# Optimization experiments

Hardware: AMD Instinct MI355X
Metric: run time of the kernel (lower is better)

Reference implementation:

```python
import jax, jax.numpy as jnp
import numpy as np

DIM = 256
HEADS = 8
HEAD_DIM = DIM // HEADS
B_, N = 8192, 49


def setup_inputs() -> dict:
    key = jax.random.key(0)
    k1, k2, k3, k4, k5, k6 = jax.random.split(key, 6)
    x = jax.random.normal(k1, (B_, N, DIM), dtype=jnp.float32)
    mask = jax.random.normal(k2, (B_, N, N), dtype=jnp.float32)
    s = 1.0 / np.sqrt(DIM)
    W_qkv = jax.random.normal(k3, (3 * DIM, DIM), dtype=jnp.float32) * s
    b_qkv = jax.random.normal(k4, (3 * DIM,), dtype=jnp.float32) * 0.02
    W_proj = jax.random.normal(k5, (DIM, DIM), dtype=jnp.float32) * s
    b_proj = jax.random.normal(k6, (DIM,), dtype=jnp.float32) * 0.02
    return {"x": x, "mask": mask, "W_qkv": W_qkv, "b_qkv": b_qkv,
            "W_proj": W_proj, "b_proj": b_proj}


def reference(x, mask, W_qkv, b_qkv, W_proj, b_proj):
    B, n, C = x.shape
    scale = HEAD_DIM ** (-0.5)
    # qkv projection: (B, N, 3C) -> (3, B, H, N, hd)
    qkv = x @ W_qkv.T + b_qkv
    qkv = qkv.reshape(B, n, 3, HEADS, HEAD_DIM).transpose(2, 0, 3, 1, 4)
    q, k, v = qkv[0], qkv[1], qkv[2]
    # scaled dot-product within each window
    attn = jnp.einsum('bhqd,bhkd->bhqk', q, k) * scale
    attn = attn + mask[:, None, :, :]  # additive window mask
    attn = jax.nn.softmax(attn, axis=-1)
    out = jnp.einsum('bhqk,bhkd->bhqd', attn, v)
    out = out.transpose(0, 2, 1, 3).reshape(B, n, C)
    return out @ W_proj.T + b_proj
```

## Files before the change

kernel.cpp:

```cpp
#include <hip/hip_runtime.h>
#include <hip/hip_bf16.h>

#define NTOK 49
#define DIMC 256

typedef __attribute__((ext_vector_type(8))) short bf16x8;
typedef __attribute__((ext_vector_type(4))) float f32x4;

static __device__ __forceinline__ unsigned pk2(float a, float b) {
    union { __hip_bfloat16 h; unsigned short u; } ua, ub;
    ua.h = __float2bfloat16(a);
    ub.h = __float2bfloat16(b);
    return (unsigned)ua.u | ((unsigned)ub.u << 16);
}

static __device__ __forceinline__ bf16x8 mkfrag(unsigned w0, unsigned w1, unsigned w2, unsigned w3) {
    union { bf16x8 v; unsigned u[4]; } t;
    t.u[0] = w0; t.u[1] = w1; t.u[2] = w2; t.u[3] = w3;
    return t.v;
}

static __device__ __forceinline__ unsigned sel2(unsigned lo, unsigned hi, int src, int ghi) {
    unsigned a = __shfl(lo, src);
    unsigned b = __shfl(hi, src);
    return ghi ? b : a;
}

__global__ void convert_weights(const float* __restrict__ wq, const float* __restrict__ wp,
                                unsigned short* __restrict__ wqb, unsigned short* __restrict__ wpb) {
    int i = blockIdx.x * 256 + threadIdx.x;
    if (i < 768 * 256) {
        union { __hip_bfloat16 h; unsigned short u; } t;
        t.h = __float2bfloat16(wq[i]);
        wqb[i] = t.u;
    }
    if (i < 256 * 256) {
        union { __hip_bfloat16 h; unsigned short u; } t;
        t.h = __float2bfloat16(wp[i]);
        wpb[i] = t.u;
    }
}

__launch_bounds__(512, 2)
__global__ void win_attn_fused(const float* __restrict__ x, const float* __restrict__ mask,
                               const unsigned short* __restrict__ wqb, const float* __restrict__ bqkv,
                               const unsigned short* __restrict__ wpb, const float* __restrict__ bproj,
                               float* __restrict__ out) {
    __shared__ __align__(16) char lds[49152];
    char* const xb = lds;
    char* const mb = lds + 32768;

    const int b = blockIdx.x;
    const int tid = threadIdx.x;
    const int lane = tid & 63;
    const int wid = tid >> 6;
    const int c = lane & 15;
    const int g = lane >> 4;

    const f32x4 fzero = {0.f, 0.f, 0.f, 0.f};

    {
        const float* xw = x + (size_t)b * (NTOK * DIMC);
        #pragma unroll
        for (int it = 0; it < 8; ++it) {
            int idx = it * 512 + tid;
            int t = idx >> 6;
            int d0 = (idx & 63) * 4;
            float4 v = make_float4(0.f, 0.f, 0.f, 0.f);
            if (t < NTOK) v = *(const float4*)(xw + t * DIMC + d0);
            *(uint2*)(xb + t * 512 + ((d0 * 2) ^ ((t & 7) << 4))) =
                make_uint2(pk2(v.x, v.y), pk2(v.z, v.w));
        }
        const float* mw = mask + (size_t)b * (NTOK * NTOK);
        #pragma unroll
        for (int it = 0; it < 8; ++it) {
            int idx = it * 512 + tid;
            int q = idx >> 6;
            int key = idx & 63;
            float v;
            if (q < NTOK && key < NTOK) v = mw[q * NTOK + key];
            else v = (key >= NTOK) ? -1e30f : 0.f;
            *(float*)(mb + q * 256 + ((key * 4) ^ ((q & 7) << 4))) = v;
        }
    }
    __syncthreads();

    const int h = wid;
    const int srcA = c + 16 * ((2 * g) & 3);
    const int srcB = c + 16 * ((2 * g + 1) & 3);
    const int ghi = g >> 1;
    const float scale = 0.17677669529663687f;

    #define XFRAG(t_, kk_) (*(const bf16x8*)(xb + (t_) * 512 + ((2 * ((kk_) + 8 * g)) ^ (((t_) & 7) << 4))))

    bf16x8 vf[2][2];
    {
        f32x4 acc[4][2];
        #pragma unroll
        for (int mt = 0; mt < 4; ++mt)
            #pragma unroll
            for (int j2 = 0; j2 < 2; ++j2) acc[mt][j2] = fzero;
        #pragma unroll
        for (int ks = 0; ks < 8; ++ks) {
            int kk = ks * 32;
            bf16x8 ax[4];
            #pragma unroll
            for (int mt = 0; mt < 4; ++mt) { int t = mt * 16 + c; ax[mt] = XFRAG(t, kk); }
            #pragma unroll
            for (int j2 = 0; j2 < 2; ++j2) {
                bf16x8 wb = *(const bf16x8*)(wqb + (512 + h * 32 + j2 * 16 + c) * 256 + kk + 8 * g);
                #pragma unroll
                for (int mt = 0; mt < 4; ++mt)
                    acc[mt][j2] = __builtin_amdgcn_mfma_f32_16x16x32_bf16(ax[mt], wb, acc[mt][j2], 0, 0, 0);
            }
        }
        float bv0 = bqkv[512 + h * 32 + c];
        float bv1 = bqkv[512 + h * 32 + 16 + c];
        unsigned vpp[4][2][2];
        #pragma unroll
        for (int mt = 0; mt < 4; ++mt) {
            vpp[mt][0][0] = pk2(acc[mt][0][0] + bv0, acc[mt][0][1] + bv0);
            vpp[mt][0][1] = pk2(acc[mt][0][2] + bv0, acc[mt][0][3] + bv0);
            vpp[mt][1][0] = pk2(acc[mt][1][0] + bv1, acc[mt][1][1] + bv1);
            vpp[mt][1][1] = pk2(acc[mt][1][2] + bv1, acc[mt][1][3] + bv1);
        }
        #pragma unroll
        for (int kh = 0; kh < 2; ++kh)
            #pragma unroll
            for (int dt = 0; dt < 2; ++dt)
                vf[kh][dt] = mkfrag(sel2(vpp[2 * kh][dt][0], vpp[2 * kh + 1][dt][0], srcA, ghi),
                                    sel2(vpp[2 * kh][dt][1], vpp[2 * kh + 1][dt][1], srcA, ghi),
                                    sel2(vpp[2 * kh][dt][0], vpp[2 * kh + 1][dt][0], srcB, ghi),
                                    sel2(vpp[2 * kh][dt][1], vpp[2 * kh + 1][dt][1], srcB, ghi));
    }

    bf16x8 ka[4];
    {
        f32x4 acc[2][4];
        #pragma unroll
        for (int md = 0; md < 2; ++md)
            #pragma unroll
            for (int j2 = 0; j2 < 4; ++j2) acc[md][j2] = fzero;
        #pragma unroll
        for (int ks = 0; ks < 8; ++ks) {
            int kk = ks * 32;
            bf16x8 bx[4];
            #pragma unroll
            for (int j2 = 0; j2 < 4; ++j2) { int t = j2 * 16 + c; bx[j2] = XFRAG(t, kk); }
            #pragma unroll
            for (int md = 0; md < 2; ++md) {
                bf16x8 wa = *(const bf16x8*)(wqb + (256 + h * 32 + md * 16 + c) * 256 + kk + 8 * g);
                #pragma unroll
                for (int j2 = 0; j2 < 4; ++j2)
                    acc[md][j2] = __builtin_amdgcn_mfma_f32_16x16x32_bf16(wa, bx[j2], acc[md][j2], 0, 0, 0);
            }
        }
        unsigned kpp[2][4][2];
        #pragma unroll
        for (int md = 0; md < 2; ++md) {
            const float* bk = bqkv + 256 + h * 32 + md * 16 + 4 * g;
            float b0 = bk[0], b1 = bk[1], b2 = bk[2], b3 = bk[3];
            #pragma unroll
            for (int j2 = 0; j2 < 4; ++j2) {
                kpp[md][j2][0] = pk2(acc[md][j2][0] + b0, acc[md][j2][1] + b1);
                kpp[md][j2][1] = pk2(acc[md][j2][2] + b2, acc[md][j2][3] + b3);
            }
        }
        #pragma unroll
        for (int it = 0; it < 4; ++it)
            ka[it] = mkfrag(sel2(kpp[0][it][0], kpp[1][it][0], srcA, ghi),
                            sel2(kpp[0][it][1], kpp[1][it][1], srcA, ghi),
                            sel2(kpp[0][it][0], kpp[1][it][0], srcB, ghi),
                            sel2(kpp[0][it][1], kpp[1][it][1], srcB, ghi));
    }

    bf16x8 qf[4];
    {
        f32x4 acc[2][4];
        #pragma unroll
        for (int md = 0; md < 2; ++md)
            #pragma unroll
            for (int j2 = 0; j2 < 4; ++j2) acc[md][j2] = fzero;
        #pragma unroll
        for (int ks = 0; ks < 8; ++ks) {
            int kk = ks * 32;
            bf16x8 bx[4];
            #pragma unroll
            for (int j2 = 0; j2 < 4; ++j2) { int t = j2 * 16 + c; bx[j2] = XFRAG(t, kk); }
            #pragma unroll
            for (int md = 0; md < 2; ++md) {
                bf16x8 wa = *(const bf16x8*)(wqb + (h * 32 + md * 16 + c) * 256 + kk + 8 * g);
                #pragma unroll
                for (int j2 = 0; j2 < 4; ++j2)
                    acc[md][j2] = __builtin_amdgcn_mfma_f32_16x16x32_bf16(wa, bx[j2], acc[md][j2], 0, 0, 0);
            }
        }
        unsigned qpp[2][4][2];
        #pragma unroll
        for (int md = 0; md < 2; ++md) {
            const float* bq = bqkv + h * 32 + md * 16 + 4 * g;
            float b0 = bq[0], b1 = bq[1], b2 = bq[2], b3 = bq[3];
            #pragma unroll
            for (int j2 = 0; j2 < 4; ++j2) {
                qpp[md][j2][0] = pk2((acc[md][j2][0] + b0) * scale, (acc[md][j2][1] + b1) * scale);
                qpp[md][j2][1] = pk2((acc[md][j2][2] + b2) * scale, (acc[md][j2][3] + b3) * scale);
            }
        }
        #pragma unroll
        for (int jt = 0; jt < 4; ++jt)
            qf[jt] = mkfrag(sel2(qpp[0][jt][0], qpp[1][jt][0], srcA, ghi),
                            sel2(qpp[0][jt][1], qpp[1][jt][1], srcA, ghi),
                            sel2(qpp[0][jt][0], qpp[1][jt][0], srcB, ghi),
                            sel2(qpp[0][jt][1], qpp[1][jt][1], srcB, ghi));
    }

    f32x4 oacc[2][4];
    #pragma unroll
    for (int dt = 0; dt < 2; ++dt)
        #pragma unroll
        for (int jt = 0; jt < 4; ++jt) oacc[dt][jt] = fzero;

    #pragma unroll
    for (int jt = 0; jt < 4; ++jt) {
        float p[4][4];
        int q = jt * 16 + c;
        #pragma unroll
        for (int it = 0; it < 4; ++it) {
            f32x4 s = __builtin_amdgcn_mfma_f32_16x16x32_bf16(ka[it], qf[jt], fzero, 0, 0, 0);
            int key0 = it * 16 + g * 4;
            f32x4 mv = *(const f32x4*)(mb + q * 256 + ((key0 * 4) ^ ((q & 7) << 4)));
            #pragma unroll
            for (int r = 0; r < 4; ++r)
                p[it][r] = s[r] + mv[r];
        }
        float m = -1e30f;
        #pragma unroll
        for (int it = 0; it < 4; ++it)
            #pragma unroll
            for (int r = 0; r < 4; ++r)
                m = fmaxf(m, p[it][r]);
        m = fmaxf(m, __shfl_xor(m, 16));
        m = fmaxf(m, __shfl_xor(m, 32));
        float ssum = 0.f;
        #pragma unroll
        for (int it = 0; it < 4; ++it)
            #pragma unroll
            for (int r = 0; r < 4; ++r) {
                float e = __expf(p[it][r] - m);
                p[it][r] = e;
                ssum += e;
            }
        ssum += __shfl_xor(ssum, 16);
        ssum += __shfl_xor(ssum, 32);
        float inv = 1.0f / ssum;
        unsigned pq[4][2];
        #pragma unroll
        for (int it = 0; it < 4; ++it) {
            pq[it][0] = pk2(p[it][0] * inv, p[it][1] * inv);
            pq[it][1] = pk2(p[it][2] * inv, p[it][3] * inv);
        }
        #pragma unroll
        for (int kh = 0; kh < 2; ++kh) {
            bf16x8 pf = mkfrag(sel2(pq[2 * kh][0], pq[2 * kh + 1][0], srcA, ghi),
                               sel2(pq[2 * kh][1], pq[2 * kh + 1][1], srcA, ghi),
                               sel2(pq[2 * kh][0], pq[2 * kh + 1][0], srcB, ghi),
                               sel2(pq[2 * kh][1], pq[2 * kh + 1][1], srcB, ghi));
            #pragma unroll
            for (int dt = 0; dt < 2; ++dt)
                oacc[dt][jt] = __builtin_amdgcn_mfma_f32_16x16x32_bf16(vf[kh][dt], pf, oacc[dt][jt], 0, 0, 0);
        }
    }

    __syncthreads();

    #pragma unroll
    for (int dt = 0; dt < 2; ++dt) {
        #pragma unroll
        for (int jt = 0; jt < 4; ++jt) {
            int q = jt * 16 + c;
            int d0 = h * 32 + dt * 16 + 4 * g;
            f32x4 v = oacc[dt][jt];
            *(uint2*)(xb + q * 512 + ((2 * d0) ^ ((q & 7) << 4))) =
                make_uint2(pk2(v[0], v[1]), pk2(v[2], v[3]));
        }
    }
    __syncthreads();

    {
        f32x4 pacc[2][4];
        #pragma unroll
        for (int j = 0; j < 2; ++j)
            #pragma unroll
            for (int mt = 0; mt < 4; ++mt) pacc[j][mt] = fzero;

        #pragma unroll
        for (int ks = 0; ks < 8; ++ks) {
            int kk = ks * 32;
            bf16x8 af[4];
            #pragma unroll
            for (int mt = 0; mt < 4; ++mt) { int t = mt * 16 + c; af[mt] = XFRAG(t, kk); }
            #pragma unroll
            for (int j = 0; j < 2; ++j) {
                int o = (wid * 2 + j) * 16 + c;
                bf16x8 bfr = *(const bf16x8*)(wpb + (size_t)o * 256 + kk + 8 * g);
                #pragma unroll
                for (int mt = 0; mt < 4; ++mt)
                    pacc[j][mt] = __builtin_amdgcn_mfma_f32_16x16x32_bf16(af[mt], bfr, pacc[j][mt], 0, 0, 0);
            }
        }
        float* ob = out + (size_t)b * (NTOK * DIMC);
        #pragma unroll
        for (int j = 0; j < 2; ++j) {
            int o = (wid * 2 + j) * 16 + c;
            float bias = bproj[o];
            #pragma unroll
            for (int mt = 0; mt < 4; ++mt) {
                #pragma unroll
                for (int r = 0; r < 4; ++r) {
                    int t = mt * 16 + g * 4 + r;
                    if (t < NTOK) ob[t * DIMC + o] = pacc[j][mt][r] + bias;
                }
            }
        }
    }
    #undef XFRAG
}

extern "C" void kernel_launch(void* const* d_in, const int* in_sizes, int n_in,
                              void* d_out, int out_size, void* d_ws, size_t ws_size,
                              hipStream_t stream) {
    const float* x    = (const float*)d_in[0];
    const float* mask = (const float*)d_in[1];
    const float* wq   = (const float*)d_in[2];
    const float* bq   = (const float*)d_in[3];
    const float* wp   = (const float*)d_in[4];
    const float* bp   = (const float*)d_in[5];
    float* o = (float*)d_out;

    unsigned short* wqb = (unsigned short*)d_ws;
    unsigned short* wpb = wqb + 768 * 256;

    convert_weights<<<768, 256, 0, stream>>>(wq, wp, wqb, wpb);
    win_attn_fused<<<8192, 512, 0, stream>>>(x, mask, wqb, bq, wpb, bp, o);
}
```

Measured before the change: 884.1 us.

## Process eight windows per block with double-buffered x prefetch and direct mask loads

Each block now loops over eight windows, keeping x in a double-buffered LDS region and prefetching the next window's x into registers while the output projection runs. The mask is read directly from global memory into registers instead of being staged in LDS, and the Q and K projections share one pass over x fragments. This aims to hide global load latency and amortize block launch costs, at the cost of doubling LDS per block (likely reducing resident blocks per CU) and more register pressure.

```diff
diff --git a/kernel.cpp b/kernel.cpp
--- a/kernel.cpp
+++ b/kernel.cpp
@@ -3,6 +3,7 @@
 
 #define NTOK 49
 #define DIMC 256
+#define WPB  8
 
 typedef __attribute__((ext_vector_type(8))) short bf16x8;
 typedef __attribute__((ext_vector_type(4))) float f32x4;
@@ -43,24 +44,28 @@
 
 __launch_bounds__(512, 2)
 __global__ void win_attn_fused(const float* __restrict__ x, const float* __restrict__ mask,
-                               const unsigned short* __restrict__ wqb, const float* __restrict__ bqkv,
-                               const unsigned short* __restrict__ wpb, const float* __restrict__ bproj,
+                               const unsigned short* __restrict__ wqkv, const float* __restrict__ bqkv,
+                               const unsigned short* __restrict__ wproj, const float* __restrict__ bproj,
                                float* __restrict__ out) {
-    __shared__ __align__(16) char lds[49152];
-    char* const xb = lds;
-    char* const mb = lds + 32768;
-
-    const int b = blockIdx.x;
+    __shared__ __align__(16) char lds[98304];
+    char* const aob = lds + 65536;
+
     const int tid = threadIdx.x;
     const int lane = tid & 63;
     const int wid = tid >> 6;
     const int c = lane & 15;
     const int g = lane >> 4;
-
+    const int h = wid;
+    const int srcA = c + 16 * ((2 * g) & 3);
+    const int srcB = c + 16 * ((2 * g + 1) & 3);
+    const int ghi = g >> 1;
+    const float scale = 0.17677669529663687f;
     const f32x4 fzero = {0.f, 0.f, 0.f, 0.f};
 
+    const int b0 = blockIdx.x * WPB;
+
     {
-        const float* xw = x + (size_t)b * (NTOK * DIMC);
+        const float* xw = x + (size_t)b0 * (NTOK * DIMC);
         #pragma unroll
         for (int it = 0; it < 8; ++it) {
             int idx = it * 512 + tid;
@@ -68,262 +73,264 @@
             int d0 = (idx & 63) * 4;
             float4 v = make_float4(0.f, 0.f, 0.f, 0.f);
             if (t < NTOK) v = *(const float4*)(xw + t * DIMC + d0);
-            *(uint2*)(xb + t * 512 + ((d0 * 2) ^ ((t & 7) << 4))) =
+            *(uint2*)(lds + t * 512 + ((d0 * 2) ^ ((t & 7) << 4))) =
                 make_uint2(pk2(v.x, v.y), pk2(v.z, v.w));
-        }
-        const float* mw = mask + (size_t)b * (NTOK * NTOK);
-        #pragma unroll
-        for (int it = 0; it < 8; ++it) {
-            int idx = it * 512 + tid;
-            int q = idx >> 6;
-            int key = idx & 63;
-            float v;
-            if (q < NTOK && key < NTOK) v = mw[q * NTOK + key];
-            else v = (key >= NTOK) ? -1e30f : 0.f;
-            *(float*)(mb + q * 256 + ((key * 4) ^ ((q & 7) << 4))) = v;
         }
     }
     __syncthreads();
 
-    const int h = wid;
-    const int srcA = c + 16 * ((2 * g) & 3);
-    const int srcB = c + 16 * ((2 * g + 1) & 3);
-    const int ghi = g >> 1;
-    const float scale = 0.17677669529663687f;
-
-    #define XFRAG(t_, kk_) (*(const bf16x8*)(xb + (t_) * 512 + ((2 * ((kk_) + 8 * g)) ^ (((t_) & 7) << 4))))
-
-    bf16x8 vf[2][2];
-    {
-        f32x4 acc[4][2];
+    #pragma unroll 1
+    for (int w = 0; w < WPB; ++w) {
+        const int b = b0 + w;
+        char* const xb = lds + (w & 1) * 32768;
+        char* const xn = lds + ((w & 1) ^ 1) * 32768;
+
+        #define XFR(base_, t_, kk_) \
+            (*(const bf16x8*)((base_) + (t_) * 512 + ((2 * ((kk_) + 8 * g)) ^ (((t_) & 7) << 4))))
+
+        bf16x8 ka[4], qf[4];
+        {
+            f32x4 aK[2][4], aQ[2][4];
+            #pragma unroll
+            for (int md = 0; md < 2; ++md)
+                #pragma unroll
+                for (int j2 = 0; j2 < 4; ++j2) { aK[md][j2] = fzero; aQ[md][j2] = fzero; }
+            #pragma unroll
+            for (int ks = 0; ks < 8; ++ks) {
+                int kk = ks * 32;
+                bf16x8 bx[4];
+                #pragma unroll
+                for (int j2 = 0; j2 < 4; ++j2) { int t = j2 * 16 + c; bx[j2] = XFR(xb, t, kk); }
+                #pragma unroll
+                for (int md = 0; md < 2; ++md) {
+                    bf16x8 wK = *(const bf16x8*)(wqkv + (256 + h * 32 + md * 16 + c) * 256 + kk + 8 * g);
+                    bf16x8 wQ = *(const bf16x8*)(wqkv + (h * 32 + md * 16 + c) * 256 + kk + 8 * g);
+                    #pragma unroll
+                    for (int j2 = 0; j2 < 4; ++j2) {
+                        aK[md][j2] = __builtin_amdgcn_mfma_f32_16x16x32_bf16(wK, bx[j2], aK[md][j2], 0, 0, 0);
+                        aQ[md][j2] = __builtin_amdgcn_mfma_f32_16x16x32_bf16(wQ, bx[j2], aQ[md][j2], 0, 0, 0);
+                    }
+                }
+            }
+            unsigned kpp[2][4][2], qpp[2][4][2];
+            #pragma unroll
+            for (int md = 0; md < 2; ++md) {
+                const float* bk = bqkv + 256 + h * 32 + md * 16 + 4 * g;
+                float k0 = bk[0], k1 = bk[1], k2 = bk[2], k3 = bk[3];
+                const float* bq = bqkv + h * 32 + md * 16 + 4 * g;
+                float q0 = bq[0], q1 = bq[1], q2 = bq[2], q3 = bq[3];
+                #pragma unroll
+                for (int j2 = 0; j2 < 4; ++j2) {
+                    kpp[md][j2][0] = pk2(aK[md][j2][0] + k0, aK[md][j2][1] + k1);
+                    kpp[md][j2][1] = pk2(aK[md][j2][2] + k2, aK[md][j2][3] + k3);
+                    qpp[md][j2][0] = pk2((aQ[md][j2][0] + q0) * scale, (aQ[md][j2][1] + q1) * scale);
+                    qpp[md][j2][1] = pk2((aQ[md][j2][2] + q2) * scale, (aQ[md][j2][3] + q3) * scale);
+                }
+            }
+            #pragma unroll
+            for (int it = 0; it < 4; ++it) {
+                ka[it] = mkfrag(sel2(kpp[0][it][0], kpp[1][it][0], srcA, ghi),
+                                sel2(kpp[0][it][1], kpp[1][it][1], srcA, ghi),
+                                sel2(kpp[0][it][0], kpp[1][it][0], srcB, ghi),
+                                sel2(kpp[0][it][1], kpp[1][it][1], srcB, ghi));
+                qf[it] = mkfrag(sel2(qpp[0][it][0], qpp[1][it][0], srcA, ghi),
+                                sel2(qpp[0][it][1], qpp[1][it][1], srcA, ghi),
+                                sel2(qpp[0][it][0], qpp[1][it][0], srcB, ghi),
+                                sel2(qpp[0][it][1], qpp[1][it][1], srcB, ghi));
+            }
+        }
+
+        bf16x8 vf[2][2];
+        {
+            f32x4 acc[4][2];
+            #pragma unroll
+            for (int mt = 0; mt < 4; ++mt)
+                #pragma unroll
+                for (int j2 = 0; j2 < 2; ++j2) acc[mt][j2] = fzero;
+            #pragma unroll
+            for (int ks = 0; ks < 8; ++ks) {
+                int kk = ks * 32;
+                bf16x8 ax[4];
+                #pragma unroll
+                for (int mt = 0; mt < 4; ++mt) { int t = mt * 16 + c; ax[mt] = XFR(xb, t, kk); }
+                #pragma unroll
+                for (int j2 = 0; j2 < 2; ++j2) {
+                    bf16x8 wb = *(const bf16x8*)(wqkv + (512 + h * 32 + j2 * 16 + c) * 256 + kk + 8 * g);
+                    #pragma unroll
+                    for (int mt = 0; mt < 4; ++mt)
+                        acc[mt][j2] = __builtin_amdgcn_mfma_f32_16x16x32_bf16(ax[mt], wb, acc[mt][j2], 0, 0, 0);
+                }
+            }
+            float bv0 = bqkv[512 + h * 32 + c];
+            float bv1 = bqkv[512 + h * 32 + 16 + c];
+            unsigned vpp[4][2][2];
+            #pragma unroll
+            for (int mt = 0; mt < 4; ++mt) {
+                vpp[mt][0][0] = pk2(acc[mt][0][0] + bv0, acc[mt][0][1] + bv0);
+                vpp[mt][0][1] = pk2(acc[mt][0][2] + bv0, acc[mt][0][3] + bv0);
+                vpp[mt][1][0] = pk2(acc[mt][1][0] + bv1, acc[mt][1][1] + bv1);
+                vpp[mt][1][1] = pk2(acc[mt][1][2] + bv1, acc[mt][1][3] + bv1);
+            }
+            #pragma unroll
+            for (int kh = 0; kh < 2; ++kh)
+                #pragma unroll
+                for (int dt = 0; dt < 2; ++dt)
+                    vf[kh][dt] = mkfrag(sel2(vpp[2 * kh][dt][0], vpp[2 * kh + 1][dt][0], srcA, ghi),
+                                        sel2(vpp[2 * kh][dt][1], vpp[2 * kh + 1][dt][1], srcA, ghi),
+                                        sel2(vpp[2 * kh][dt][0], vpp[2 * kh + 1][dt][0], srcB, ghi),
+                                        sel2(vpp[2 * kh][dt][1], vpp[2 * kh + 1][dt][1], srcB, ghi));
+        }
+
+        f32x4 oacc[2][4];
         #pragma unroll
-        for (int mt = 0; mt < 4; ++mt)
-            #pragma unroll
-            for (int j2 = 0; j2 < 2; ++j2) acc[mt][j2] = fzero;
-        #pragma unroll
-        for (int ks = 0; ks < 8; ++ks) {
-            int kk = ks * 32;
-            bf16x8 ax[4];
-            #pragma unroll
-            for (int mt = 0; mt < 4; ++mt) { int t = mt * 16 + c; ax[mt] = XFRAG(t, kk); }
-            #pragma unroll
-            for (int j2 = 0; j2 < 2; ++j2) {
-                bf16x8 wb = *(const bf16x8*)(wqb + (512 + h * 32 + j2 * 16 + c) * 256 + kk + 8 * g);
-                #pragma unroll
-                for (int mt = 0; mt < 4; ++mt)
-                    acc[mt][j2] = __builtin_amdgcn_mfma_f32_16x16x32_bf16(ax[mt], wb, acc[mt][j2], 0, 0, 0);
-            }
-        }
-        float bv0 = bqkv[512 + h * 32 + c];
-        float bv1 = bqkv[512 + h * 32 + 16 + c];
-        unsigned vpp[4][2][2];
-        #pragma unroll
-        for (int mt = 0; mt < 4; ++mt) {
-            vpp[mt][0][0] = pk2(acc[mt][0][0] + bv0, acc[mt][0][1] + bv0);
-            vpp[mt][0][1] = pk2(acc[mt][0][2] + bv0, acc[mt][0][3] + bv0);
-            vpp[mt][1][0] = pk2(acc[mt][1][0] + bv1, acc[mt][1][1] + bv1);
-            vpp[mt][1][1] = pk2(acc[mt][1][2] + bv1, acc[mt][1][3] + bv1);
-        }
-        #pragma unroll
-        for (int kh = 0; kh < 2; ++kh)
-            #pragma unroll
-            for (int dt = 0; dt < 2; ++dt)
-                vf[kh][dt] = mkfrag(sel2(vpp[2 * kh][dt][0], vpp[2 * kh + 1][dt][0], srcA, ghi),
-                                    sel2(vpp[2 * kh][dt][1], vpp[2 * kh + 1][dt][1], srcA, ghi),
-                                    sel2(vpp[2 * kh][dt][0], vpp[2 * kh + 1][dt][0], srcB, ghi),
-                                    sel2(vpp[2 * kh][dt][1], vpp[2 * kh + 1][dt][1], srcB, ghi));
-    }
-
-    bf16x8 ka[4];
-    {
-        f32x4 acc[2][4];
-        #pragma unroll
-        for (int md = 0; md < 2; ++md)
-            #pragma unroll
-            for (int j2 = 0; j2 < 4; ++j2) acc[md][j2] = fzero;
-        #pragma unroll
-        for (int ks = 0; ks < 8; ++ks) {
-            int kk = ks * 32;
-            bf16x8 bx[4];
-            #pragma unroll
-            for (int j2 = 0; j2 < 4; ++j2) { int t = j2 * 16 + c; bx[j2] = XFRAG(t, kk); }
-            #pragma unroll
-            for (int md = 0; md < 2; ++md) {
-                bf16x8 wa = *(const bf16x8*)(wqb + (256 + h * 32 + md * 16 + c) * 256 + kk + 8 * g);
-                #pragma unroll
-                for (int j2 = 0; j2 < 4; ++j2)
-                    acc[md][j2] = __builtin_amdgcn_mfma_f32_16x16x32_bf16(wa, bx[j2], acc[md][j2], 0, 0, 0);
-            }
-        }
-        unsigned kpp[2][4][2];
-        #pragma unroll
-        for (int md = 0; md < 2; ++md) {
-            const float* bk = bqkv + 256 + h * 32 + md * 16 + 4 * g;
-            float b0 = bk[0], b1 = bk[1], b2 = bk[2], b3 = bk[3];
-            #pragma unroll
-            for (int j2 = 0; j2 < 4; ++j2) {
-                kpp[md][j2][0] = pk2(acc[md][j2][0] + b0, acc[md][j2][1] + b1);
-                kpp[md][j2][1] = pk2(acc[md][j2][2] + b2, acc[md][j2][3] + b3);
-            }
-        }
-        #pragma unroll
-        for (int it = 0; it < 4; ++it)
-            ka[it] = mkfrag(sel2(kpp[0][it][0], kpp[1][it][0], srcA, ghi),
-                            sel2(kpp[0][it][1], kpp[1][it][1], srcA, ghi),
-                            sel2(kpp[0][it][0], kpp[1][it][0], srcB, ghi),
-                            sel2(kpp[0][it][1], kpp[1][it][1], srcB, ghi));
-    }
-
-    bf16x8 qf[4];
-    {
-        f32x4 acc[2][4];
-        #pragma unroll
-        for (int md = 0; md < 2; ++md)
-            #pragma unroll
-            for (int j2 = 0; j2 < 4; ++j2) acc[md][j2] = fzero;
-        #pragma unroll
-        for (int ks = 0; ks < 8; ++ks) {
-            int kk = ks * 32;
-            bf16x8 bx[4];
-            #pragma unroll
-            for (int j2 = 0; j2 < 4; ++j2) { int t = j2 * 16 + c; bx[j2] = XFRAG(t, kk); }
-            #pragma unroll
-            for (int md = 0; md < 2; ++md) {
-                bf16x8 wa = *(const bf16x8*)(wqb + (h * 32 + md * 16 + c) * 256 + kk + 8 * g);
-                #pragma unroll
-                for (int j2 = 0; j2 < 4; ++j2)
-                    acc[md][j2] = __builtin_amdgcn_mfma_f32_16x16x32_bf16(wa, bx[j2], acc[md][j2], 0, 0, 0);
-            }
-        }
-        unsigned qpp[2][4][2];
-        #pragma unroll
-        for (int md = 0; md < 2; ++md) {
-            const float* bq = bqkv + h * 32 + md * 16 + 4 * g;
-            float b0 = bq[0], b1 = bq[1], b2 = bq[2], b3 = bq[3];
-            #pragma unroll
-            for (int j2 = 0; j2 < 4; ++j2) {
-                qpp[md][j2][0] = pk2((acc[md][j2][0] + b0) * scale, (acc[md][j2][1] + b1) * scale);
-                qpp[md][j2][1] = pk2((acc[md][j2][2] + b2) * scale, (acc[md][j2][3] + b3) * scale);
-            }
-        }
-        #pragma unroll
-        for (int jt = 0; jt < 4; ++jt)
-            qf[jt] = mkfrag(sel2(qpp[0][jt][0], qpp[1][jt][0], srcA, ghi),
-                            sel2(qpp[0][jt][1], qpp[1][jt][1], srcA, ghi),
-                            sel2(qpp[0][jt][0], qpp[1][jt][0], srcB, ghi),
-                            sel2(qpp[0][jt][1], qpp[1][jt][1], srcB, ghi));
-    }
-
-    f32x4 oacc[2][4];
-    #pragma unroll
-    for (int dt = 0; dt < 2; ++dt)
-        #pragma unroll
-        for (int jt = 0; jt < 4; ++jt) oacc[dt][jt] = fzero;
-
-    #pragma unroll
-    for (int jt = 0; jt < 4; ++jt) {
-        float p[4][4];
-        int q = jt * 16 + c;
-        #pragma unroll
-        for (int it = 0; it < 4; ++it) {
-            f32x4 s = __builtin_amdgcn_mfma_f32_16x16x32_bf16(ka[it], qf[jt], fzero, 0, 0, 0);
-            int key0 = it * 16 + g * 4;
-            f32x4 mv = *(const f32x4*)(mb + q * 256 + ((key0 * 4) ^ ((q & 7) << 4)));
-            #pragma unroll
-            for (int r = 0; r < 4; ++r)
-                p[it][r] = s[r] + mv[r];
-        }
-        float m = -1e30f;
-        #pragma unroll
-        for (int it = 0; it < 4; ++it)
-            #pragma unroll
-            for (int r = 0; r < 4; ++r)
-                m = fmaxf(m, p[it][r]);
-        m = fmaxf(m, __shfl_xor(m, 16));
-        m = fmaxf(m, __shfl_xor(m, 32));
-        float ssum = 0.f;
-        #pragma unroll
-        for (int it = 0; it < 4; ++it)
-            #pragma unroll
-            for (int r = 0; r < 4; ++r) {
-                float e = __expf(p[it][r] - m);
-                p[it][r] = e;
-                ssum += e;
-            }
-        ssum += __shfl_xor(ssum, 16);
-        ssum += __shfl_xor(ssum, 32);
-        float inv = 1.0f / ssum;
-        unsigned pq[4][2];
-        #pragma unroll
-        for (int it = 0; it < 4; ++it) {
-            pq[it][0] = pk2(p[it][0] * inv, p[it][1] * inv);
-            pq[it][1] = pk2(p[it][2] * inv, p[it][3] * inv);
-        }
-        #pragma unroll
-        for (int kh = 0; kh < 2; ++kh) {
-            bf16x8 pf = mkfrag(sel2(pq[2 * kh][0], pq[2 * kh + 1][0], srcA, ghi),
-                               sel2(pq[2 * kh][1], pq[2 * kh + 1][1], srcA, ghi),
-                               sel2(pq[2 * kh][0], pq[2 * kh + 1][0], srcB, ghi),
-                               sel2(pq[2 * kh][1], pq[2 * kh + 1][1], srcB, ghi));
-            #pragma unroll
-            for (int dt = 0; dt < 2; ++dt)
-                oacc[dt][jt] = __builtin_amdgcn_mfma_f32_16x16x32_bf16(vf[kh][dt], pf, oacc[dt][jt], 0, 0, 0);
-        }
-    }
-
-    __syncthreads();
-
-    #pragma unroll
-    for (int dt = 0; dt < 2; ++dt) {
+        for (int dt = 0; dt < 2; ++dt)
+            #pragma unroll
+            for (int jt = 0; jt < 4; ++jt) oacc[dt][jt] = fzero;
+
+        const float* mw = mask + (size_t)b * (NTOK * NTOK);
         #pragma unroll
         for (int jt = 0; jt < 4; ++jt) {
             int q = jt * 16 + c;
-            int d0 = h * 32 + dt * 16 + 4 * g;
-            f32x4 v = oacc[dt][jt];
-            *(uint2*)(xb + q * 512 + ((2 * d0) ^ ((q & 7) << 4))) =
-                make_uint2(pk2(v[0], v[1]), pk2(v[2], v[3]));
-        }
-    }
-    __syncthreads();
-
-    {
-        f32x4 pacc[2][4];
+            int qc = (q < NTOK) ? q : (NTOK - 1);
+            const float* mrow = mw + qc * NTOK;
+            f32x4 mv0 = *(const f32x4*)(mrow + 0 + g * 4);
+            f32x4 mv1 = *(const f32x4*)(mrow + 16 + g * 4);
+            f32x4 mv2 = *(const f32x4*)(mrow + 32 + g * 4);
+            float m48 = mrow[48];
+            float p[4][4];
+            {
+                f32x4 s = __builtin_amdgcn_mfma_f32_16x16x32_bf16(ka[0], qf[jt], fzero, 0, 0, 0);
+                #pragma unroll
+                for (int r = 0; r < 4; ++r) p[0][r] = s[r] + mv0[r];
+            }
+            {
+                f32x4 s = __builtin_amdgcn_mfma_f32_16x16x32_bf16(ka[1], qf[jt], fzero, 0, 0, 0);
+                #pragma unroll
+                for (int r = 0; r < 4; ++r) p[1][r] = s[r] + mv1[r];
+            }
+            {
+                f32x4 s = __builtin_amdgcn_mfma_f32_16x16x32_bf16(ka[2], qf[jt], fzero, 0, 0, 0);
+                #pragma unroll
+                for (int r = 0; r < 4; ++r) p[2][r] = s[r] + mv2[r];
+            }
+            {
+                f32x4 s = __builtin_amdgcn_mfma_f32_16x16x32_bf16(ka[3], qf[jt], fzero, 0, 0, 0);
+                #pragma unroll
+                for (int r = 0; r < 4; ++r)
+                    p[3][r] = (g == 0 && r == 0) ? (s[0] + m48) : -1e30f;
+            }
+            float m = -1e30f;
+            #pragma unroll
+            for (int it = 0; it < 4; ++it)
+                #pragma unroll
+                for (int r = 0; r < 4; ++r) m = fmaxf(m, p[it][r]);
+            m = fmaxf(m, __shfl_xor(m, 16));
+            m = fmaxf(m, __shfl_xor(m, 32));
+            float ssum = 0.f;
+            #pragma unroll
+            for (int it = 0; it < 4; ++it)
+                #pragma unroll
+                for (int r = 0; r < 4; ++r) {
+                    float e = __expf(p[it][r] - m);
+                    p[it][r] = e;
+                    ssum += e;
+                }
+            ssum += __shfl_xor(ssum, 16);
+            ssum += __shfl_xor(ssum, 32);
+            float inv = 1.0f / ssum;
+            unsigned pq[4][2];
+            #pragma unroll
+            for (int it = 0; it < 4; ++it) {
+                pq[it][0] = pk2(p[it][0] * inv, p[it][1] * inv);
+                pq[it][1] = pk2(p[it][2] * inv, p[it][3] * inv);
+            }
+            #pragma unroll
+            for (int kh = 0; kh < 2; ++kh) {
+                bf16x8 pf = mkfrag(sel2(pq[2 * kh][0], pq[2 * kh + 1][0], srcA, ghi),
+                                   sel2(pq[2 * kh][1], pq[2 * kh + 1][1], srcA, ghi),
+                                   sel2(pq[2 * kh][0], pq[2 * kh + 1][0], srcB, ghi),
+                                   sel2(pq[2 * kh][1], pq[2 * kh + 1][1], srcB, ghi));
+                #pragma unroll
+                for (int dt = 0; dt < 2; ++dt)
+                    oacc[dt][jt] = __builtin_amdgcn_mfma_f32_16x16x32_bf16(vf[kh][dt], pf, oacc[dt][jt], 0, 0, 0);
+            }
+        }
+
         #pragma unroll
-        for (int j = 0; j < 2; ++j)
-            #pragma unroll
-            for (int mt = 0; mt < 4; ++mt) pacc[j][mt] = fzero;
-
-        #pragma unroll
-        for (int ks = 0; ks < 8; ++ks) {
-            int kk = ks * 32;
-            bf16x8 af[4];
-            #pragma unroll
-            for (int mt = 0; mt < 4; ++mt) { int t = mt * 16 + c; af[mt] = XFRAG(t, kk); }
+        for (int dt = 0; dt < 2; ++dt) {
+            #pragma unroll
+            for (int jt = 0; jt < 4; ++jt) {
+                int q = jt * 16 + c;
+                int d0 = h * 32 + dt * 16 + 4 * g;
+                f32x4 v = oacc[dt][jt];
+                *(uint2*)(aob + q * 512 + ((2 * d0) ^ ((q & 7) << 4))) =
+                    make_uint2(pk2(v[0], v[1]), pk2(v[2], v[3]));
+            }
+        }
+        __syncthreads();
+
+        float4 px[8];
+        const bool pf_on = (w + 1 < WPB);
+        if (pf_on) {
+            const float* xw2 = x + (size_t)(b + 1) * (NTOK * DIMC);
+            #pragma unroll
+            for (int it = 0; it < 8; ++it) {
+                int idx = it * 512 + tid;
+                int t = idx >> 6;
+                int d0 = (idx & 63) * 4;
+                px[it] = make_float4(0.f, 0.f, 0.f, 0.f);
+                if (t < NTOK) px[it] = *(const float4*)(xw2 + t * DIMC + d0);
+            }
+        }
+        {
+            f32x4 pacc[2][4];
+            #pragma unroll
+            for (int j = 0; j < 2; ++j)
+                #pragma unroll
+                for (int mt = 0; mt < 4; ++mt) pacc[j][mt] = fzero;
+            #pragma unroll
+            for (int ks = 0; ks < 8; ++ks) {
+                int kk = ks * 32;
+                bf16x8 af[4];
+                #pragma unroll
+                for (int mt = 0; mt < 4; ++mt) { int t = mt * 16 + c; af[mt] = XFR(aob, t, kk); }
+                #pragma unroll
+                for (int j = 0; j < 2; ++j) {
+                    int o = (wid * 2 + j) * 16 + c;
+                    bf16x8 bfr = *(const bf16x8*)(wproj + (size_t)o * 256 + kk + 8 * g);
+                    #pragma unroll
+                    for (int mt = 0; mt < 4; ++mt)
+                        pacc[j][mt] = __builtin_amdgcn_mfma_f32_16x16x32_bf16(af[mt], bfr, pacc[j][mt], 0, 0, 0);
+                }
+            }
+            float* ob = out + (size_t)b * (NTOK * DIMC);
             #pragma unroll
             for (int j = 0; j < 2; ++j) {
                 int o = (wid * 2 + j) * 16 + c;
-                bf16x8 bfr = *(const bf16x8*)(wpb + (size_t)o * 256 + kk + 8 * g);
-                #pragma unroll
-                for (int mt = 0; mt < 4; ++mt)
-                    pacc[j][mt] = __builtin_amdgcn_mfma_f32_16x16x32_bf16(af[mt], bfr, pacc[j][mt], 0, 0, 0);
-            }
-        }
-        float* ob = out + (size_t)b * (NTOK * DIMC);
-        #pragma unroll
-        for (int j = 0; j < 2; ++j) {
-            int o = (wid * 2 + j) * 16 + c;
-            float bias = bproj[o];
-            #pragma unroll
-            for (int mt = 0; mt < 4; ++mt) {
-                #pragma unroll
-                for (int r = 0; r < 4; ++r) {
-                    int t = mt * 16 + g * 4 + r;
-                    if (t < NTOK) ob[t * DIMC + o] = pacc[j][mt][r] + bias;
-                }
-            }
-        }
+                float bias = bproj[o];
+                #pragma unroll
+                for (int mt = 0; mt < 4; ++mt) {
+                    #pragma unroll
+                    for (int r = 0; r < 4; ++r) {
+                        int t = mt * 16 + g * 4 + r;
+                        if (t < NTOK) ob[t * DIMC + o] = pacc[j][mt][r] + bias;
+                    }
+                }
+            }
+        }
+        if (pf_on) {
+            #pragma unroll
+            for (int it = 0; it < 8; ++it) {
+                int idx = it * 512 + tid;
+                int t = idx >> 6;
+                int d0 = (idx & 63) * 4;
+                *(uint2*)(xn + t * 512 + ((d0 * 2) ^ ((t & 7) << 4))) =
+                    make_uint2(pk2(px[it].x, px[it].y), pk2(px[it].z, px[it].w));
+            }
+        }
+        __syncthreads();
+        #undef XFR
     }
-    #undef XFRAG
 }
 
 extern "C" void kernel_launch(void* const* d_in, const int* in_sizes, int n_in,
@@ -341,5 +348,5 @@
     unsigned short* wpb = wqb + 768 * 256;
 
     convert_weights<<<768, 256, 0, stream>>>(wq, wp, wqb, wpb);
-    win_attn_fused<<<8192, 512, 0, stream>>>(x, mask, wqb, bq, wpb, bp, o);
-}
+    win_attn_fused<<<8192 / WPB, 512, 0, stream>>>(x, mask, wqb, bq, wpb, bp, o);
+}
```

Result: slower. 1.496 ms (+69.2%).
